# Performance work log

Measured on AMD Instinct MI355X. Metric: run time of the kernel, lower is better.

The kernel has to match this reference:

```python
import jax, jax.numpy as jnp
import numpy as np


def setup_inputs() -> dict:
    key = jax.random.key(0)
    ks = jax.random.split(key, 12)
    B, C, H, W = 8, 256, 64, 64
    inter = C // 8
    s = 0.05  # weight scale keeps q.k logits in a stable softmax range
    f32 = jnp.float32
    x = jax.random.normal(ks[0], (B, C, H, W), f32)
    Wq = jax.random.normal(ks[1], (inter, C), f32) * s
    bq = jnp.zeros((inter,), f32)
    Wk = jax.random.normal(ks[2], (inter, C), f32) * s
    bk = jnp.zeros((inter,), f32)
    Wv = jax.random.normal(ks[3], (C, C), f32) * s
    bv = jnp.zeros((C,), f32)
    gamma = jnp.full((1,), 0.5, f32)  # learnable residual scale (init 0 in torch; 0.5 exercises the path)
    Wg1 = jax.random.normal(ks[4], (inter, C), f32) * s
    bg1 = jnp.zeros((inter,), f32)
    Wg2 = jax.random.normal(ks[5], (C, inter), f32) * s
    bg2 = jnp.zeros((C,), f32)
    return {"x": x, "Wq": Wq, "bq": bq, "Wk": Wk, "bk": bk, "Wv": Wv, "bv": bv,
            "gamma": gamma, "Wg1": Wg1, "bg1": bg1, "Wg2": Wg2, "bg2": bg2}


def reference(x, Wq, bq, Wk, bk, Wv, bv, gamma, Wg1, bg1, Wg2, bg2):
    B, C, H, W = x.shape
    N = H * W
    xf = x.reshape(B, C, N)  # [B,C,N]
    # 1x1 convs == per-pixel linear projections
    q = jnp.einsum('oc,bcn->bon', Wq, xf) + bq[None, :, None]  # [B,inter,N]
    k = jnp.einsum('oc,bcn->bon', Wk, xf) + bk[None, :, None]  # [B,inter,N]
    v = jnp.einsum('oc,bcn->bon', Wv, xf) + bv[None, :, None]  # [B,C,N]
    # attention[b,n,m] = softmax_m( q[b,:,n] . k[b,:,m] )
    attn = jax.nn.softmax(jnp.einsum('bin,bim->bnm', q, k), axis=-1)  # [B,N,N]
    # out[b,c,n] = sum_m v[b,c,m] * attn[b,n,m]
    out = jnp.einsum('bcm,bnm->bcn', v, attn)  # [B,C,N]
    out = gamma[0] * out + xf
    # gated global pooling branch: GAP -> 1x1 conv -> ReLU -> 1x1 conv -> Sigmoid
    gp = xf.mean(axis=-1)  # [B,C]
    h = jax.nn.relu(jnp.einsum('oc,bc->bo', Wg1, gp) + bg1)  # [B,inter]
    ga = jax.nn.sigmoid(jnp.einsum('co,bo->bc', Wg2, h) + bg2)  # [B,C]
    out = out * ga[:, :, None] + out
    return out.reshape(B, C, H, W)
```

## Files before the change

### kernel.cpp

```cpp
#include <hip/hip_runtime.h>

typedef unsigned short u16;
typedef unsigned int   u32;
typedef short s16x4 __attribute__((ext_vector_type(4)));
typedef u16 u16x4 __attribute__((ext_vector_type(4)));
typedef u16 u16x8 __attribute__((ext_vector_type(8)));
typedef __bf16 bf16x8 __attribute__((ext_vector_type(8)));
typedef float f32x4 __attribute__((ext_vector_type(4)));
typedef float f32x2 __attribute__((ext_vector_type(2)));
typedef u32 u32x2v __attribute__((ext_vector_type(2)));
typedef u32 u32x4v __attribute__((ext_vector_type(4)));

#define NB 8
#define NC 256
#define NI 32
#define NN 4096
#define LOG2E 1.4426950408889634f
#define POFF 64.0f

#define OW_Q   0
#define OB_Q   8192
#define OW_K   8224
#define OB_K   16416
#define OW_V   16448
#define OB_V   81984
#define OGAM   82240
#define OW_G1  82248
#define OB_G1  90440
#define OW_G2  90472
#define OB_G2  98664
#define WTOT   98920

__device__ __forceinline__ float bf2f(u16 v) {
    u32 u = ((u32)v) << 16;
    return __builtin_bit_cast(float, u);
}
__device__ __forceinline__ u16 f2bf(float f) {
    u32 u = __builtin_bit_cast(u32, f);
    u32 lsb = (u >> 16) & 1u;
    u += 0x7fffu + lsb;
    return (u16)(u >> 16);
}
__device__ __forceinline__ u32 cvtpk_bf16(float lo, float hi) {
    u32 r;
    asm("v_cvt_pk_bf16_f32 %0, %1, %2" : "=v"(r) : "v"(lo), "v"(hi));
    return r;
}
__device__ __forceinline__ u16 f2bf_hw(float f) {
    u32 r;
    asm("v_cvt_pk_bf16_f32 %0, %1, %1" : "=v"(r) : "v"(f));
    return (u16)r;
}
__device__ __forceinline__ void permswap32(u32& a, u32& b) {
#if __has_builtin(__builtin_amdgcn_permlane32_swap)
    auto r = __builtin_amdgcn_permlane32_swap(a, b, false, false);
    a = (u32)r[0]; b = (u32)r[1];
#else
    int ln = (int)(threadIdx.x & 63);
    u32 a2 = (u32)__shfl_xor((int)a, 32, 64);
    u32 b2 = (u32)__shfl_xor((int)b, 32, 64);
    u32 na = (ln < 32) ? a : b2;
    u32 nb = (ln < 32) ? a2 : b;
    a = na; b = nb;
#endif
}
__device__ __forceinline__ void permswap16(u32& a, u32& b) {
#if __has_builtin(__builtin_amdgcn_permlane16_swap)
    auto r = __builtin_amdgcn_permlane16_swap(a, b, false, false);
    a = (u32)r[0]; b = (u32)r[1];
#else
    int q = (int)((threadIdx.x >> 4) & 1);
    u32 az = (u32)__shfl_xor((int)a, 16, 64);
    u32 bz = (u32)__shfl_xor((int)b, 16, 64);
    u32 na = q ? bz : a;
    u32 nb = q ? b  : az;
    a = na; b = nb;
#endif
}
__device__ __forceinline__ bool is_f32_mode(const void* graw) {
    return ((const u16*)graw)[0] == 0;
}

__global__ __launch_bounds__(256) void convert_kernel(
    const void* x,  const void* Wq, const void* bq, const void* Wk, const void* bk,
    const void* Wv, const void* bv, const void* gamma, const void* Wg1, const void* bg1,
    const void* Wg2, const void* bg2, float* __restrict__ xf, float* __restrict__ wbuf,
    u16* __restrict__ wbf, float* __restrict__ gp)
{
    bool f32m = is_f32_mode(gamma);
    int blk = blockIdx.x, t = threadIdx.x;
    if (blk < 2048) {
        int base = blk * 4096 + t * 16;
        float s = 0.f;
        if (f32m) {
            const float* xs = (const float*)x;
#pragma unroll
            for (int k = 0; k < 4; ++k) {
                f32x4 a = *(const f32x4*)(xs + base + k * 4);
                s += (a[0] + a[1]) + (a[2] + a[3]);
            }
        } else {
            const u16* xs = (const u16*)x;
#pragma unroll
            for (int k = 0; k < 2; ++k) {
                u16x8 a = *(const u16x8*)(xs + base + k * 8);
                f32x4 lo, hi;
#pragma unroll
                for (int j = 0; j < 4; ++j) { lo[j] = bf2f(a[j]); hi[j] = bf2f(a[4 + j]); }
                *(f32x4*)(xf + base + k * 8)     = lo;
                *(f32x4*)(xf + base + k * 8 + 4) = hi;
                s += (lo[0]+lo[1])+(lo[2]+lo[3]) + (hi[0]+hi[1])+(hi[2]+hi[3]);
            }
        }
#pragma unroll
        for (int off = 1; off <= 32; off <<= 1) s += __shfl_xor(s, off, 64);
        __shared__ float ws[4];
        if ((t & 63) == 0) ws[t >> 6] = s;
        __syncthreads();
        if (t == 0) gp[blk] = (ws[0] + ws[1] + ws[2] + ws[3]) * (1.0f / NN);
        return;
    }
    if (blk < 2080) {
        int tid = (blk - 2048) * 256 + t;
        const int off[12] = {OW_Q, OB_Q, OW_K, OB_K, OW_V, OB_V, OGAM, OW_G1, OB_G1, OW_G2, OB_G2, WTOT};
        const int len[11] = {8192, 32, 8192, 32, 65536, 256, 1, 8192, 32, 8192, 256};
        const void* srcs[11] = {Wq, bq, Wk, bk, Wv, bv, gamma, Wg1, bg1, Wg2, bg2};
        for (int w = tid; w < WTOT; w += 32 * 256) {
            int seg = 0;
#pragma unroll
            for (int i = 1; i < 11; ++i) if (w >= off[i]) seg = i;
            int idx = w - off[seg];
            float val = 0.f;
            if (idx < len[seg])
                val = f32m ? ((const float*)srcs[seg])[idx] : bf2f(((const u16*)srcs[seg])[idx]);
            wbuf[w] = val;
        }
        return;
    }
    int tid = (blk - 2080) * 256 + t;
    for (int w = tid; w < 320 * 256; w += 10 * 256) {
        int row = w >> 8, c = w & 255;
        const void* src; int idx; float scale = 1.f;
        if (row < 32)      { src = Wq; idx = row * 256 + c; scale = LOG2E; }
        else if (row < 64) { src = Wk; idx = (row - 32) * 256 + c; }
        else               { src = Wv; idx = (row - 64) * 256 + c; }
        float val = f32m ? ((const float*)src)[idx] : bf2f(((const u16*)src)[idx]);
        wbf[w] = f2bf(val * scale);
    }
}

__global__ __launch_bounds__(256) void proj_kernel(
    const void* xr, const float* __restrict__ xf, const void* graw,
    const float* __restrict__ wbuf, const u16* __restrict__ wbf,
    u16* __restrict__ qt, u16* __restrict__ kt, u16* __restrict__ v)
{
    __shared__ __attribute__((aligned(16))) u16 xs[64][264];

    const float* X = is_f32_mode(graw) ? (const float*)xr : xf;

    int t    = threadIdx.x;
    int lane = t & 63;
    int wave = t >> 6;
    int b    = blockIdx.x >> 6;
    int m0   = (blockIdx.x & 63) << 6;
    int l15  = lane & 15;
    int quad = lane >> 4;

    {
        const float* xb = X + (size_t)b * NC * NN + m0 + lane;
        int c0 = wave * 64;
#pragma unroll
        for (int ci = 0; ci < 64; ci += 4) {
            int c = c0 + ci;
            float a0 = xb[(size_t)(c    ) * NN];
            float a1 = xb[(size_t)(c + 1) * NN];
            float a2 = xb[(size_t)(c + 2) * NN];
            float a3 = xb[(size_t)(c + 3) * NN];
            u32x2v p2;
            p2.x = cvtpk_bf16(a0, a1);
            p2.y = cvtpk_bf16(a2, a3);
            *(u32x2v*)&xs[lane][c] = p2;
        }
    }
    __syncthreads();

    const f32x4 zero4 = {};
    f32x4 acc[5][4];
#pragma unroll
    for (int i = 0; i < 5; ++i)
#pragma unroll
        for (int mt = 0; mt < 4; ++mt) acc[i][mt] = zero4;

    int obase = wave * 80;
    const u16* wb = wbf + (size_t)(obase + l15) * 256 + quad * 8;

    bf16x8 af[5];
#pragma unroll
    for (int i = 0; i < 5; ++i)
        af[i] = *(const bf16x8*)(wb + (size_t)(i * 16) * 256);

#pragma unroll
    for (int kc = 0; kc < 8; ++kc) {
        bf16x8 afn[5], bfr[4];
        if (kc < 7) {
#pragma unroll
            for (int i = 0; i < 5; ++i)
                afn[i] = *(const bf16x8*)(wb + (size_t)(i * 16) * 256 + (kc + 1) * 32);
        }
#pragma unroll
        for (int mt = 0; mt < 4; ++mt)
            bfr[mt] = *(const bf16x8*)&xs[mt * 16 + l15][kc * 32 + quad * 8];
#pragma unroll
        for (int i = 0; i < 5; ++i)
#pragma unroll
            for (int mt = 0; mt < 4; ++mt)
                acc[i][mt] = __builtin_amdgcn_mfma_f32_16x16x32_bf16(af[i], bfr[mt], acc[i][mt], 0, 0, 0);
        if (kc < 7) {
#pragma unroll
            for (int i = 0; i < 5; ++i) af[i] = afn[i];
        }
    }

    __syncthreads();

    if (wave == 0) {
#pragma unroll
        for (int i = 0; i < 4; ++i) {
#pragma unroll
            for (int mt = 0; mt < 4; ++mt) {
                float tv[4];
#pragma unroll
                for (int r = 0; r < 4; ++r) {
                    int o = i * 16 + quad * 4 + r;
                    float bias = (o < 32) ? LOG2E * wbuf[OB_Q + o] : wbuf[OB_K + o - 32];
                    tv[r] = acc[i][mt][r] + bias;
                }
                u32x2v p2;
                p2.x = cvtpk_bf16(tv[0], tv[1]);
                p2.y = cvtpk_bf16(tv[2], tv[3]);
                *(u32x2v*)&xs[mt * 16 + l15][i * 16 + quad * 4] = p2;
            }
        }
        int m = m0 + lane;
        u16* qrow = qt + (size_t)(b * NN + m) * NI;
        u16* krow = kt + (size_t)(b * NN + m) * NI;
#pragma unroll
        for (int j = 0; j < 4; ++j) *(u16x8*)(qrow + j * 8) = *(const u16x8*)&xs[lane][j * 8];
#pragma unroll
        for (int j = 0; j < 4; ++j) *(u16x8*)(krow + j * 8) = *(const u16x8*)&xs[lane][32 + j * 8];
#pragma unroll
        for (int mt = 0; mt < 4; ++mt) {
#pragma unroll
            for (int r = 0; r < 4; ++r) {
                int c = quad * 4 + r;
                v[(size_t)(b * NC + c) * NN + m0 + mt * 16 + l15] = f2bf_hw(acc[4][mt][r] + wbuf[OB_V + c]);
            }
        }
    } else {
#pragma unroll
        for (int i = 0; i < 5; ++i) {
#pragma unroll
            for (int mt = 0; mt < 4; ++mt) {
#pragma unroll
                for (int r = 0; r < 4; ++r) {
                    int c = wave * 80 + i * 16 + quad * 4 + r - 64;
                    v[(size_t)(b * NC + c) * NN + m0 + mt * 16 + l15] = f2bf_hw(acc[i][mt][r] + wbuf[OB_V + c]);
                }
            }
        }
    }
}

__global__ __launch_bounds__(256) void gate_kernel(
    const float* __restrict__ gp, const float* __restrict__ wbuf, float* __restrict__ gmul)
{
    int b = blockIdx.x;
    int t = threadIdx.x;
    __shared__ float gps[NC];
    __shared__ float hs[NI];
    gps[t] = gp[b * NC + t];
    __syncthreads();
    if (t < NI) {
        float a = wbuf[OB_G1 + t];
        for (int c = 0; c < NC; ++c) a += wbuf[OW_G1 + t * NC + c] * gps[c];
        hs[t] = a > 0.f ? a : 0.f;
    }
    __syncthreads();
    float a = wbuf[OB_G2 + t];
#pragma unroll
    for (int i = 0; i < NI; ++i) a += wbuf[OW_G2 + t * NI + i] * hs[i];
    float sig = 1.f / (1.f + __expf(-a));
    gmul[b * NC + t] = 1.f + sig;
}

__global__ __launch_bounds__(512, 4) void flash_kernel(
    const u16* __restrict__ qt, const u16* __restrict__ kt, const u16* __restrict__ v,
    const void* xr, const float* __restrict__ xf, const void* graw,
    const float* __restrict__ wbuf, const float* __restrict__ gmul, void* outp)
{
    __shared__ __attribute__((aligned(16))) u16 vs[2][2][NC][40];

    bool f32m = is_f32_mode(graw);
    const float* X = f32m ? (const float*)xr : xf;

    int t    = threadIdx.x;
    int lane = t & 63;
    int wave = t >> 6;
    int b    = blockIdx.x & 7;
    int nblk = (blockIdx.x >> 3) << 6;
    int n0   = nblk + (wave >> 2) * 32;
    int c0   = (wave & 3) * 64;
    int l15  = lane & 15;
    int quad = lane >> 4;

    const f32x4 mneg = {-POFF, -POFF, -POFF, -POFF};

    bf16x8 qf[2];
#pragma unroll
    for (int n16 = 0; n16 < 2; ++n16)
        qf[n16] = *(const bf16x8*)(qt + (size_t)(b * NN + n0 + n16 * 16 + l15) * NI + quad * 8);

    f32x4 acc[2][4];
#pragma unroll
    for (int n16 = 0; n16 < 2; ++n16)
#pragma unroll
        for (int ct = 0; ct < 4; ++ct) acc[n16][ct] = f32x4{};
    f32x2 psum2[2] = {};

    int sc = t >> 2;
    int sm = (t & 3) * 8;
    const u16* vb0 = v + (size_t)(b * NC + sc) * NN + sm;
    const u16* vb1 = v + (size_t)(b * NC + sc + 128) * NN + sm;
    const u16* ktb = kt + (size_t)(b * NN + l15) * NI + quad * 8;

    u16x8 sr0, sr1, sr2, sr3;
    sr0 = *(const u16x8*)(vb0);        sr1 = *(const u16x8*)(vb1);
    sr2 = *(const u16x8*)(vb0 + 32);   sr3 = *(const u16x8*)(vb1 + 32);
    *(u16x8*)&vs[0][0][sc][sm]       = sr0;
    *(u16x8*)&vs[0][0][sc + 128][sm] = sr1;
    *(u16x8*)&vs[0][1][sc][sm]       = sr2;
    *(u16x8*)&vs[0][1][sc + 128][sm] = sr3;
    sr0 = *(const u16x8*)(vb0 + 64);   sr1 = *(const u16x8*)(vb1 + 64);
    sr2 = *(const u16x8*)(vb0 + 96);   sr3 = *(const u16x8*)(vb1 + 96);
    bf16x8 ktA[2], ktB[2];
    ktA[0] = *(const bf16x8*)(ktb);
    ktA[1] = *(const bf16x8*)(ktb + (size_t)16 * NI);
    ktB[0] = *(const bf16x8*)(ktb + (size_t)32 * NI);
    ktB[1] = *(const bf16x8*)(ktb + (size_t)48 * NI);
    __syncthreads();

    for (int it = 0; it < 64; ++it) {
        int p = it & 1;
        bool wmore = (it < 63);
        bool lmore = (it < 62);

        if (wmore) {
            *(u16x8*)&vs[p ^ 1][0][sc][sm]       = sr0;
            *(u16x8*)&vs[p ^ 1][0][sc + 128][sm] = sr1;
            *(u16x8*)&vs[p ^ 1][1][sc][sm]       = sr2;
            *(u16x8*)&vs[p ^ 1][1][sc + 128][sm] = sr3;
        }
        if (lmore) {
            int cb = it * 64 + 128;
            sr0 = *(const u16x8*)(vb0 + cb);
            sr1 = *(const u16x8*)(vb1 + cb);
            sr2 = *(const u16x8*)(vb0 + cb + 32);
            sr3 = *(const u16x8*)(vb1 + cb + 32);
        }

#pragma unroll
        for (int h = 0; h < 2; ++h) {
            bf16x8* ktX = (h == 0) ? ktA : ktB;

            f32x4 sf[2][2];
#pragma unroll
            for (int mt = 0; mt < 2; ++mt)
#pragma unroll
                for (int n16 = 0; n16 < 2; ++n16)
                    sf[n16][mt] = __builtin_amdgcn_mfma_f32_16x16x32_bf16(ktX[mt], qf[n16], mneg, 0, 0, 0);

            bf16x8 va8[4];
#pragma unroll
            for (int ct = 0; ct < 4; ++ct)
                va8[ct] = *(const bf16x8*)&vs[p][h][c0 + ct * 16 + l15][quad * 8];

            if (wmore) {
                int mg = it * 64 + 64 + h * 32;
                ktX[0] = *(const bf16x8*)(ktb + (size_t)mg * NI);
                ktX[1] = *(const bf16x8*)(ktb + (size_t)(mg + 16) * NI);
            }

            bf16x8 pfr8[2];
#pragma unroll
            for (int n16 = 0; n16 < 2; ++n16) {
                float pp[2][4];
#pragma unroll
                for (int mt = 0; mt < 2; ++mt)
#pragma unroll
                    for (int r = 0; r < 4; ++r)
                        pp[mt][r] = __builtin_amdgcn_exp2f(sf[n16][mt][r]);
                f32x2 t0; t0.x = pp[0][0]; t0.y = pp[0][1];
                f32x2 t1; t1.x = pp[0][2]; t1.y = pp[0][3];
                f32x2 t2; t2.x = pp[1][0]; t2.y = pp[1][1];
                f32x2 t3; t3.x = pp[1][2]; t3.y = pp[1][3];
                psum2[n16] += (t0 + t1) + (t2 + t3);
                u32 A0 = cvtpk_bf16(pp[0][0], pp[0][1]);
                u32 A1 = cvtpk_bf16(pp[0][2], pp[0][3]);
                u32 B0 = cvtpk_bf16(pp[1][0], pp[1][1]);
                u32 B1 = cvtpk_bf16(pp[1][2], pp[1][3]);
                permswap32(A0, B0); permswap16(A0, B0);
                permswap32(A1, B1); permswap16(A1, B1);
                u32x4v f; f.x = A0; f.y = A1; f.z = B0; f.w = B1;
                pfr8[n16] = __builtin_bit_cast(bf16x8, f);
            }

#pragma unroll
            for (int ct = 0; ct < 4; ++ct)
#pragma unroll
                for (int n16 = 0; n16 < 2; ++n16)
                    acc[n16][ct] = __builtin_amdgcn_mfma_f32_16x16x32_bf16(va8[ct], pfr8[n16], acc[n16][ct], 0, 0, 0);
        }

        __syncthreads();
    }

    float inv[2];
#pragma unroll
    for (int n16 = 0; n16 < 2; ++n16) {
        float s = psum2[n16].x + psum2[n16].y;
        s += __shfl_xor(s, 16, 64);
        s += __shfl_xor(s, 32, 64);
        inv[n16] = 1.f / s;
    }
    float gam = wbuf[OGAM];

#pragma unroll
    for (int n16 = 0; n16 < 2; ++n16) {
        int n = n0 + n16 * 16 + l15;
#pragma unroll
        for (int ct = 0; ct < 4; ++ct) {
            int cb = c0 + ct * 16 + quad * 4;
            f32x4 gm4 = *(const f32x4*)&gmul[b * NC + cb];
#pragma unroll
            for (int r = 0; r < 4; ++r) {
                size_t off = (size_t)(b * NC + cb + r) * NN + n;
                float val = (gam * acc[n16][ct][r] * inv[n16] + X[off]) * gm4[r];
                if (f32m) ((float*)outp)[off] = val;
                else      ((u16*)outp)[off]  = f2bf_hw(val);
            }
        }
    }
}

extern "C" void kernel_launch(void* const* d_in, const int* in_sizes, int n_in,
                              void* d_out, int out_size, void* d_ws, size_t ws_size,
                              hipStream_t stream)
{
    const void* x     = d_in[0];
    const void* Wq    = d_in[1];
    const void* bq    = d_in[2];
    const void* Wk    = d_in[3];
    const void* bk    = d_in[4];
    const void* Wv    = d_in[5];
    const void* bvp   = d_in[6];
    const void* gamma = d_in[7];
    const void* Wg1   = d_in[8];
    const void* bg1   = d_in[9];
    const void* Wg2   = d_in[10];
    const void* bg2   = d_in[11];

    char* ws = (char*)d_ws;
    float* xf   = (float*)ws;
    float* wbuf = (float*)(ws + 33554432);
    u16*   qt   = (u16*)  (ws + 33951744);
    u16*   kt   = (u16*)  (ws + 36048896);
    u16*   v    = (u16*)  (ws + 38146048);
    float* gp   = (float*)(ws + 54923264);
    float* gmul = (float*)(ws + 54931456);
    u16*   wbf  = (u16*)  (ws + 54939648);

    convert_kernel<<<2090, 256, 0, stream>>>(x, Wq, bq, Wk, bk, Wv, bvp, gamma,
                                             Wg1, bg1, Wg2, bg2, xf, wbuf, wbf, gp);
    proj_kernel<<<NB * 64, 256, 0, stream>>>(x, xf, gamma, wbuf, wbf, qt, kt, v);
    gate_kernel<<<NB, 256, 0, stream>>>(gp, wbuf, gmul);
    flash_kernel<<<NB * 64, 512, 0, stream>>>(qt, kt, v, x, xf, gamma, wbuf, gmul, d_out);
}
```

Baseline: 270.0 us.

## Retile flash waves to 16 rows x 128 channels; drop bf16 x staging copy

The flash kernel's per-wave tile changes from 32 query rows by 64 channels to 16 query rows by 128 channels. Each wave now computes one QK score tile per key block instead of two, so exp2, softmax-sum and pack work per wave halves, while each wave reads twice as many V fragments from LDS. Separately, the bf16 path no longer writes an fp32 copy of x in the pooling kernel; the projection and epilogue read bf16 x directly. The inputs here are fp32, so the default run mostly sees the retiling, which trades fewer redundant exponentials for more LDS traffic per wave.

```diff
diff --git a/kernel.cpp b/kernel.cpp
--- a/kernel.cpp
+++ b/kernel.cpp
@@ -104,12 +104,8 @@
 #pragma unroll
             for (int k = 0; k < 2; ++k) {
                 u16x8 a = *(const u16x8*)(xs + base + k * 8);
-                f32x4 lo, hi;
-#pragma unroll
-                for (int j = 0; j < 4; ++j) { lo[j] = bf2f(a[j]); hi[j] = bf2f(a[4 + j]); }
-                *(f32x4*)(xf + base + k * 8)     = lo;
-                *(f32x4*)(xf + base + k * 8 + 4) = hi;
-                s += (lo[0]+lo[1])+(lo[2]+lo[3]) + (hi[0]+hi[1])+(hi[2]+hi[3]);
+#pragma unroll
+                for (int j = 0; j < 8; ++j) s += bf2f(a[j]);
             }
         }
 #pragma unroll
@@ -156,7 +152,7 @@
 {
     __shared__ __attribute__((aligned(16))) u16 xs[64][264];
 
-    const float* X = is_f32_mode(graw) ? (const float*)xr : xf;
+    bool f32m = is_f32_mode(graw);
 
     int t    = threadIdx.x;
     int lane = t & 63;
@@ -167,19 +163,33 @@
     int quad = lane >> 4;
 
     {
-        const float* xb = X + (size_t)b * NC * NN + m0 + lane;
         int c0 = wave * 64;
-#pragma unroll
-        for (int ci = 0; ci < 64; ci += 4) {
-            int c = c0 + ci;
-            float a0 = xb[(size_t)(c    ) * NN];
-            float a1 = xb[(size_t)(c + 1) * NN];
-            float a2 = xb[(size_t)(c + 2) * NN];
-            float a3 = xb[(size_t)(c + 3) * NN];
-            u32x2v p2;
-            p2.x = cvtpk_bf16(a0, a1);
-            p2.y = cvtpk_bf16(a2, a3);
-            *(u32x2v*)&xs[lane][c] = p2;
+        if (f32m) {
+            const float* xb = (const float*)xr + (size_t)b * NC * NN + m0 + lane;
+#pragma unroll
+            for (int ci = 0; ci < 64; ci += 4) {
+                int c = c0 + ci;
+                float a0 = xb[(size_t)(c    ) * NN];
+                float a1 = xb[(size_t)(c + 1) * NN];
+                float a2 = xb[(size_t)(c + 2) * NN];
+                float a3 = xb[(size_t)(c + 3) * NN];
+                u32x2v p2;
+                p2.x = cvtpk_bf16(a0, a1);
+                p2.y = cvtpk_bf16(a2, a3);
+                *(u32x2v*)&xs[lane][c] = p2;
+            }
+        } else {
+            const u16* xb = (const u16*)xr + (size_t)b * NC * NN + m0 + lane;
+#pragma unroll
+            for (int ci = 0; ci < 64; ci += 4) {
+                int c = c0 + ci;
+                u16x4 p4;
+                p4[0] = xb[(size_t)(c    ) * NN];
+                p4[1] = xb[(size_t)(c + 1) * NN];
+                p4[2] = xb[(size_t)(c + 2) * NN];
+                p4[3] = xb[(size_t)(c + 3) * NN];
+                *(u16x4*)&xs[lane][c] = p4;
+            }
         }
     }
     __syncthreads();
@@ -301,31 +311,25 @@
     __shared__ __attribute__((aligned(16))) u16 vs[2][2][NC][40];
 
     bool f32m = is_f32_mode(graw);
-    const float* X = f32m ? (const float*)xr : xf;
 
     int t    = threadIdx.x;
     int lane = t & 63;
     int wave = t >> 6;
     int b    = blockIdx.x & 7;
     int nblk = (blockIdx.x >> 3) << 6;
-    int n0   = nblk + (wave >> 2) * 32;
-    int c0   = (wave & 3) * 64;
+    int n0   = nblk + (wave >> 1) * 16;
+    int c0   = (wave & 1) * 128;
     int l15  = lane & 15;
     int quad = lane >> 4;
 
     const f32x4 mneg = {-POFF, -POFF, -POFF, -POFF};
 
-    bf16x8 qf[2];
-#pragma unroll
-    for (int n16 = 0; n16 < 2; ++n16)
-        qf[n16] = *(const bf16x8*)(qt + (size_t)(b * NN + n0 + n16 * 16 + l15) * NI + quad * 8);
-
-    f32x4 acc[2][4];
-#pragma unroll
-    for (int n16 = 0; n16 < 2; ++n16)
-#pragma unroll
-        for (int ct = 0; ct < 4; ++ct) acc[n16][ct] = f32x4{};
-    f32x2 psum2[2] = {};
+    bf16x8 qf = *(const bf16x8*)(qt + (size_t)(b * NN + n0 + l15) * NI + quad * 8);
+
+    f32x4 acc[8];
+#pragma unroll
+    for (int ct = 0; ct < 8; ++ct) acc[ct] = f32x4{};
+    f32x2 psum2 = {};
 
     int sc = t >> 2;
     int sm = (t & 3) * 8;
@@ -372,16 +376,14 @@
         for (int h = 0; h < 2; ++h) {
             bf16x8* ktX = (h == 0) ? ktA : ktB;
 
-            f32x4 sf[2][2];
+            f32x4 sf[2];
 #pragma unroll
             for (int mt = 0; mt < 2; ++mt)
-#pragma unroll
-                for (int n16 = 0; n16 < 2; ++n16)
-                    sf[n16][mt] = __builtin_amdgcn_mfma_f32_16x16x32_bf16(ktX[mt], qf[n16], mneg, 0, 0, 0);
-
-            bf16x8 va8[4];
-#pragma unroll
-            for (int ct = 0; ct < 4; ++ct)
+                sf[mt] = __builtin_amdgcn_mfma_f32_16x16x32_bf16(ktX[mt], qf, mneg, 0, 0, 0);
+
+            bf16x8 va8[8];
+#pragma unroll
+            for (int ct = 0; ct < 8; ++ct)
                 va8[ct] = *(const bf16x8*)&vs[p][h][c0 + ct * 16 + l15][quad * 8];
 
             if (wmore) {
@@ -390,64 +392,52 @@
                 ktX[1] = *(const bf16x8*)(ktb + (size_t)(mg + 16) * NI);
             }
 
-            bf16x8 pfr8[2];
-#pragma unroll
-            for (int n16 = 0; n16 < 2; ++n16) {
-                float pp[2][4];
-#pragma unroll
-                for (int mt = 0; mt < 2; ++mt)
-#pragma unroll
-                    for (int r = 0; r < 4; ++r)
-                        pp[mt][r] = __builtin_amdgcn_exp2f(sf[n16][mt][r]);
-                f32x2 t0; t0.x = pp[0][0]; t0.y = pp[0][1];
-                f32x2 t1; t1.x = pp[0][2]; t1.y = pp[0][3];
-                f32x2 t2; t2.x = pp[1][0]; t2.y = pp[1][1];
-                f32x2 t3; t3.x = pp[1][2]; t3.y = pp[1][3];
-                psum2[n16] += (t0 + t1) + (t2 + t3);
-                u32 A0 = cvtpk_bf16(pp[0][0], pp[0][1]);
-                u32 A1 = cvtpk_bf16(pp[0][2], pp[0][3]);
-                u32 B0 = cvtpk_bf16(pp[1][0], pp[1][1]);
-                u32 B1 = cvtpk_bf16(pp[1][2], pp[1][3]);
-                permswap32(A0, B0); permswap16(A0, B0);
-                permswap32(A1, B1); permswap16(A1, B1);
-                u32x4v f; f.x = A0; f.y = A1; f.z = B0; f.w = B1;
-                pfr8[n16] = __builtin_bit_cast(bf16x8, f);
-            }
-
-#pragma unroll
-            for (int ct = 0; ct < 4; ++ct)
-#pragma unroll
-                for (int n16 = 0; n16 < 2; ++n16)
-                    acc[n16][ct] = __builtin_amdgcn_mfma_f32_16x16x32_bf16(va8[ct], pfr8[n16], acc[n16][ct], 0, 0, 0);
+            float pp[2][4];
+#pragma unroll
+            for (int mt = 0; mt < 2; ++mt)
+#pragma unroll
+                for (int r = 0; r < 4; ++r)
+                    pp[mt][r] = __builtin_amdgcn_exp2f(sf[mt][r]);
+            f32x2 t0; t0.x = pp[0][0]; t0.y = pp[0][1];
+            f32x2 t1; t1.x = pp[0][2]; t1.y = pp[0][3];
+            f32x2 t2; t2.x = pp[1][0]; t2.y = pp[1][1];
+            f32x2 t3; t3.x = pp[1][2]; t3.y = pp[1][3];
+            psum2 += (t0 + t1) + (t2 + t3);
+            u32 A0 = cvtpk_bf16(pp[0][0], pp[0][1]);
+            u32 A1 = cvtpk_bf16(pp[0][2], pp[0][3]);
+            u32 B0 = cvtpk_bf16(pp[1][0], pp[1][1]);
+            u32 B1 = cvtpk_bf16(pp[1][2], pp[1][3]);
+            permswap32(A0, B0); permswap16(A0, B0);
+            permswap32(A1, B1); permswap16(A1, B1);
+            u32x4v f; f.x = A0; f.y = A1; f.z = B0; f.w = B1;
+            bf16x8 pfr8 = __builtin_bit_cast(bf16x8, f);
+
+#pragma unroll
+            for (int ct = 0; ct < 8; ++ct)
+                acc[ct] = __builtin_amdgcn_mfma_f32_16x16x32_bf16(va8[ct], pfr8, acc[ct], 0, 0, 0);
         }
 
         __syncthreads();
     }
 
-    float inv[2];
-#pragma unroll
-    for (int n16 = 0; n16 < 2; ++n16) {
-        float s = psum2[n16].x + psum2[n16].y;
-        s += __shfl_xor(s, 16, 64);
-        s += __shfl_xor(s, 32, 64);
-        inv[n16] = 1.f / s;
-    }
+    float s = psum2.x + psum2.y;
+    s += __shfl_xor(s, 16, 64);
+    s += __shfl_xor(s, 32, 64);
+    float inv = 1.f / s;
     float gam = wbuf[OGAM];
-
-#pragma unroll
-    for (int n16 = 0; n16 < 2; ++n16) {
-        int n = n0 + n16 * 16 + l15;
-#pragma unroll
-        for (int ct = 0; ct < 4; ++ct) {
-            int cb = c0 + ct * 16 + quad * 4;
-            f32x4 gm4 = *(const f32x4*)&gmul[b * NC + cb];
-#pragma unroll
-            for (int r = 0; r < 4; ++r) {
-                size_t off = (size_t)(b * NC + cb + r) * NN + n;
-                float val = (gam * acc[n16][ct][r] * inv[n16] + X[off]) * gm4[r];
-                if (f32m) ((float*)outp)[off] = val;
-                else      ((u16*)outp)[off]  = f2bf_hw(val);
-            }
+    int n = n0 + l15;
+
+#pragma unroll
+    for (int ct = 0; ct < 8; ++ct) {
+        int cb = c0 + ct * 16 + quad * 4;
+        f32x4 gm4 = *(const f32x4*)&gmul[b * NC + cb];
+#pragma unroll
+        for (int r = 0; r < 4; ++r) {
+            size_t off = (size_t)(b * NC + cb + r) * NN + n;
+            float xv = f32m ? ((const float*)xr)[off] : bf2f(((const u16*)xr)[off]);
+            float val = (gam * acc[ct][r] * inv + xv) * gm4[r];
+            if (f32m) ((float*)outp)[off] = val;
+            else      ((u16*)outp)[off]  = f2bf_hw(val);
         }
     }
 }
```

New measurement: 257.9 us. 1.05x faster.

## Split key halves across waves to cut redundant softmax work, reduce partials via LDS

Applied to the files above, without the earlier changes.

Repartitions flash-attention waves so each wave handles one 32-key half and 128 channels instead of both halves and 64 channels. This halves the duplicated QK MFMA and exp2 work per wave, and a shared-memory reduction merges the partial accumulators and denominators at the end. It also removes the bf16-to-f32 staging copy of x, so later kernels read bf16 input directly. In exchange, accumulator registers double, which may pressure occupancy, and an extra LDS epilogue is added.

```diff
diff --git a/kernel.cpp b/kernel.cpp
--- a/kernel.cpp
+++ b/kernel.cpp
@@ -104,12 +104,8 @@
 #pragma unroll
             for (int k = 0; k < 2; ++k) {
                 u16x8 a = *(const u16x8*)(xs + base + k * 8);
-                f32x4 lo, hi;
-#pragma unroll
-                for (int j = 0; j < 4; ++j) { lo[j] = bf2f(a[j]); hi[j] = bf2f(a[4 + j]); }
-                *(f32x4*)(xf + base + k * 8)     = lo;
-                *(f32x4*)(xf + base + k * 8 + 4) = hi;
-                s += (lo[0]+lo[1])+(lo[2]+lo[3]) + (hi[0]+hi[1])+(hi[2]+hi[3]);
+#pragma unroll
+                for (int j = 0; j < 8; ++j) s += bf2f(a[j]);
             }
         }
 #pragma unroll
@@ -156,7 +152,7 @@
 {
     __shared__ __attribute__((aligned(16))) u16 xs[64][264];
 
-    const float* X = is_f32_mode(graw) ? (const float*)xr : xf;
+    bool f32m = is_f32_mode(graw);
 
     int t    = threadIdx.x;
     int lane = t & 63;
@@ -167,19 +163,33 @@
     int quad = lane >> 4;
 
     {
-        const float* xb = X + (size_t)b * NC * NN + m0 + lane;
         int c0 = wave * 64;
-#pragma unroll
-        for (int ci = 0; ci < 64; ci += 4) {
-            int c = c0 + ci;
-            float a0 = xb[(size_t)(c    ) * NN];
-            float a1 = xb[(size_t)(c + 1) * NN];
-            float a2 = xb[(size_t)(c + 2) * NN];
-            float a3 = xb[(size_t)(c + 3) * NN];
-            u32x2v p2;
-            p2.x = cvtpk_bf16(a0, a1);
-            p2.y = cvtpk_bf16(a2, a3);
-            *(u32x2v*)&xs[lane][c] = p2;
+        if (f32m) {
+            const float* xb = (const float*)xr + (size_t)b * NC * NN + m0 + lane;
+#pragma unroll
+            for (int ci = 0; ci < 64; ci += 4) {
+                int c = c0 + ci;
+                float a0 = xb[(size_t)(c    ) * NN];
+                float a1 = xb[(size_t)(c + 1) * NN];
+                float a2 = xb[(size_t)(c + 2) * NN];
+                float a3 = xb[(size_t)(c + 3) * NN];
+                u32x2v p2;
+                p2.x = cvtpk_bf16(a0, a1);
+                p2.y = cvtpk_bf16(a2, a3);
+                *(u32x2v*)&xs[lane][c] = p2;
+            }
+        } else {
+            const u16* xb = (const u16*)xr + (size_t)b * NC * NN + m0 + lane;
+#pragma unroll
+            for (int ci = 0; ci < 64; ci += 4) {
+                int c = c0 + ci;
+                u16x4 p4;
+                p4[0] = xb[(size_t)(c    ) * NN];
+                p4[1] = xb[(size_t)(c + 1) * NN];
+                p4[2] = xb[(size_t)(c + 2) * NN];
+                p4[3] = xb[(size_t)(c + 3) * NN];
+                *(u16x4*)&xs[lane][c] = p4;
+            }
         }
     }
     __syncthreads();
@@ -301,15 +311,17 @@
     __shared__ __attribute__((aligned(16))) u16 vs[2][2][NC][40];
 
     bool f32m = is_f32_mode(graw);
-    const float* X = f32m ? (const float*)xr : xf;
 
     int t    = threadIdx.x;
     int lane = t & 63;
     int wave = t >> 6;
+    int mg   = wave & 1;
+    int cg   = (wave >> 1) & 1;
+    int ng   = wave >> 2;
     int b    = blockIdx.x & 7;
     int nblk = (blockIdx.x >> 3) << 6;
-    int n0   = nblk + (wave >> 2) * 32;
-    int c0   = (wave & 3) * 64;
+    int n0   = nblk + ng * 32;
+    int c0   = cg * 128;
     int l15  = lane & 15;
     int quad = lane >> 4;
 
@@ -320,11 +332,11 @@
     for (int n16 = 0; n16 < 2; ++n16)
         qf[n16] = *(const bf16x8*)(qt + (size_t)(b * NN + n0 + n16 * 16 + l15) * NI + quad * 8);
 
-    f32x4 acc[2][4];
+    f32x4 acc[2][8];
 #pragma unroll
     for (int n16 = 0; n16 < 2; ++n16)
 #pragma unroll
-        for (int ct = 0; ct < 4; ++ct) acc[n16][ct] = f32x4{};
+        for (int ct = 0; ct < 8; ++ct) acc[n16][ct] = f32x4{};
     f32x2 psum2[2] = {};
 
     int sc = t >> 2;
@@ -342,11 +354,9 @@
     *(u16x8*)&vs[0][1][sc + 128][sm] = sr3;
     sr0 = *(const u16x8*)(vb0 + 64);   sr1 = *(const u16x8*)(vb1 + 64);
     sr2 = *(const u16x8*)(vb0 + 96);   sr3 = *(const u16x8*)(vb1 + 96);
-    bf16x8 ktA[2], ktB[2];
-    ktA[0] = *(const bf16x8*)(ktb);
-    ktA[1] = *(const bf16x8*)(ktb + (size_t)16 * NI);
-    ktB[0] = *(const bf16x8*)(ktb + (size_t)32 * NI);
-    ktB[1] = *(const bf16x8*)(ktb + (size_t)48 * NI);
+    bf16x8 ktA[2];
+    ktA[0] = *(const bf16x8*)(ktb + (size_t)(mg * 32     ) * NI);
+    ktA[1] = *(const bf16x8*)(ktb + (size_t)(mg * 32 + 16) * NI);
     __syncthreads();
 
     for (int it = 0; it < 64; ++it) {
@@ -368,85 +378,101 @@
             sr3 = *(const u16x8*)(vb1 + cb + 32);
         }
 
-#pragma unroll
-        for (int h = 0; h < 2; ++h) {
-            bf16x8* ktX = (h == 0) ? ktA : ktB;
-
-            f32x4 sf[2][2];
+        f32x4 sf[2][2];
+#pragma unroll
+        for (int mt = 0; mt < 2; ++mt)
+#pragma unroll
+            for (int n16 = 0; n16 < 2; ++n16)
+                sf[n16][mt] = __builtin_amdgcn_mfma_f32_16x16x32_bf16(ktA[mt], qf[n16], mneg, 0, 0, 0);
+
+        if (wmore) {
+            int mgn = (it + 1) * 64 + mg * 32;
+            ktA[0] = *(const bf16x8*)(ktb + (size_t)(mgn     ) * NI);
+            ktA[1] = *(const bf16x8*)(ktb + (size_t)(mgn + 16) * NI);
+        }
+
+        bf16x8 pfr8[2];
+#pragma unroll
+        for (int n16 = 0; n16 < 2; ++n16) {
+            float pp[2][4];
 #pragma unroll
             for (int mt = 0; mt < 2; ++mt)
 #pragma unroll
-                for (int n16 = 0; n16 < 2; ++n16)
-                    sf[n16][mt] = __builtin_amdgcn_mfma_f32_16x16x32_bf16(ktX[mt], qf[n16], mneg, 0, 0, 0);
-
-            bf16x8 va8[4];
-#pragma unroll
-            for (int ct = 0; ct < 4; ++ct)
-                va8[ct] = *(const bf16x8*)&vs[p][h][c0 + ct * 16 + l15][quad * 8];
-
-            if (wmore) {
-                int mg = it * 64 + 64 + h * 32;
-                ktX[0] = *(const bf16x8*)(ktb + (size_t)mg * NI);
-                ktX[1] = *(const bf16x8*)(ktb + (size_t)(mg + 16) * NI);
-            }
-
-            bf16x8 pfr8[2];
-#pragma unroll
-            for (int n16 = 0; n16 < 2; ++n16) {
-                float pp[2][4];
-#pragma unroll
-                for (int mt = 0; mt < 2; ++mt)
-#pragma unroll
-                    for (int r = 0; r < 4; ++r)
-                        pp[mt][r] = __builtin_amdgcn_exp2f(sf[n16][mt][r]);
-                f32x2 t0; t0.x = pp[0][0]; t0.y = pp[0][1];
-                f32x2 t1; t1.x = pp[0][2]; t1.y = pp[0][3];
-                f32x2 t2; t2.x = pp[1][0]; t2.y = pp[1][1];
-                f32x2 t3; t3.x = pp[1][2]; t3.y = pp[1][3];
-                psum2[n16] += (t0 + t1) + (t2 + t3);
-                u32 A0 = cvtpk_bf16(pp[0][0], pp[0][1]);
-                u32 A1 = cvtpk_bf16(pp[0][2], pp[0][3]);
-                u32 B0 = cvtpk_bf16(pp[1][0], pp[1][1]);
-                u32 B1 = cvtpk_bf16(pp[1][2], pp[1][3]);
-                permswap32(A0, B0); permswap16(A0, B0);
-                permswap32(A1, B1); permswap16(A1, B1);
-                u32x4v f; f.x = A0; f.y = A1; f.z = B0; f.w = B1;
-                pfr8[n16] = __builtin_bit_cast(bf16x8, f);
-            }
-
-#pragma unroll
-            for (int ct = 0; ct < 4; ++ct)
-#pragma unroll
-                for (int n16 = 0; n16 < 2; ++n16)
-                    acc[n16][ct] = __builtin_amdgcn_mfma_f32_16x16x32_bf16(va8[ct], pfr8[n16], acc[n16][ct], 0, 0, 0);
+                for (int r = 0; r < 4; ++r)
+                    pp[mt][r] = __builtin_amdgcn_exp2f(sf[n16][mt][r]);
+            f32x2 t0; t0.x = pp[0][0]; t0.y = pp[0][1];
+            f32x2 t1; t1.x = pp[0][2]; t1.y = pp[0][3];
+            f32x2 t2; t2.x = pp[1][0]; t2.y = pp[1][1];
+            f32x2 t3; t3.x = pp[1][2]; t3.y = pp[1][3];
+            psum2[n16] += (t0 + t1) + (t2 + t3);
+            u32 A0 = cvtpk_bf16(pp[0][0], pp[0][1]);
+            u32 A1 = cvtpk_bf16(pp[0][2], pp[0][3]);
+            u32 B0 = cvtpk_bf16(pp[1][0], pp[1][1]);
+            u32 B1 = cvtpk_bf16(pp[1][2], pp[1][3]);
+            permswap32(A0, B0); permswap16(A0, B0);
+            permswap32(A1, B1); permswap16(A1, B1);
+            u32x4v f; f.x = A0; f.y = A1; f.z = B0; f.w = B1;
+            pfr8[n16] = __builtin_bit_cast(bf16x8, f);
+        }
+
+#pragma unroll
+        for (int ct = 0; ct < 8; ++ct) {
+            bf16x8 va = *(const bf16x8*)&vs[p][mg][c0 + ct * 16 + l15][quad * 8];
+            acc[0][ct] = __builtin_amdgcn_mfma_f32_16x16x32_bf16(va, pfr8[0], acc[0][ct], 0, 0, 0);
+            acc[1][ct] = __builtin_amdgcn_mfma_f32_16x16x32_bf16(va, pfr8[1], acc[1][ct], 0, 0, 0);
         }
 
         __syncthreads();
     }
 
-    float inv[2];
+    float* sbuf = (float*)&vs[0][0][0][0];
+    float* dlp  = (float*)((char*)&vs[0][0][0][0] + 70656);
+    int pid = wave >> 1;
+
+    float sden[2];
 #pragma unroll
     for (int n16 = 0; n16 < 2; ++n16) {
         float s = psum2[n16].x + psum2[n16].y;
         s += __shfl_xor(s, 16, 64);
         s += __shfl_xor(s, 32, 64);
-        inv[n16] = 1.f / s;
-    }
-    float gam = wbuf[OGAM];
-
-#pragma unroll
-    for (int n16 = 0; n16 < 2; ++n16) {
-        int n = n0 + n16 * 16 + l15;
-#pragma unroll
-        for (int ct = 0; ct < 4; ++ct) {
-            int cb = c0 + ct * 16 + quad * 4;
-            f32x4 gm4 = *(const f32x4*)&gmul[b * NC + cb];
-#pragma unroll
-            for (int r = 0; r < 4; ++r) {
-                size_t off = (size_t)(b * NC + cb + r) * NN + n;
-                float val = (gam * acc[n16][ct][r] * inv[n16] + X[off]) * gm4[r];
-                if (f32m) ((float*)outp)[off] = val;
-                else      ((u16*)outp)[off]  = f2bf_hw(val);
+        sden[n16] = s;
+    }
+    if (quad == 0) {
+        dlp[(wave * 2 + 0) * 16 + l15] = sden[0];
+        dlp[(wave * 2 + 1) * 16 + l15] = sden[1];
+    }
+    if (mg == 1) {
+#pragma unroll
+        for (int n16 = 0; n16 < 2; ++n16)
+#pragma unroll
+            for (int ct = 0; ct < 8; ++ct)
+                *(f32x4*)&sbuf[pid * 4352 + lane * 68 + n16 * 32 + ct * 4] = acc[n16][ct];
+    }
+    __syncthreads();
+    if (mg == 0) {
+        float inv[2];
+#pragma unroll
+        for (int n16 = 0; n16 < 2; ++n16)
+            inv[n16] = 1.f / (dlp[(wave * 2 + n16) * 16 + l15] +
+                              dlp[((wave + 1) * 2 + n16) * 16 + l15]);
+        float gam = wbuf[OGAM];
+#pragma unroll
+        for (int n16 = 0; n16 < 2; ++n16) {
+            int n = n0 + n16 * 16 + l15;
+#pragma unroll
+            for (int ct = 0; ct < 8; ++ct) {
+                f32x4 part = *(const f32x4*)&sbuf[pid * 4352 + lane * 68 + n16 * 32 + ct * 4];
+                int cb = c0 + ct * 16 + quad * 4;
+                f32x4 gm4 = *(const f32x4*)&gmul[b * NC + cb];
+#pragma unroll
+                for (int r = 0; r < 4; ++r) {
+                    size_t off = (size_t)(b * NC + cb + r) * NN + n;
+                    float a  = acc[n16][ct][r] + part[r];
+                    float xv = f32m ? ((const float*)xr)[off] : bf2f(((const u16*)xr)[off]);
+                    float val = (gam * a * inv[n16] + xv) * gm4[r];
+                    if (f32m) ((float*)outp)[off] = val;
+                    else      ((u16*)outp)[off]  = f2bf_hw(val);
+                }
             }
         }
     }
```

Result: slower. 279.6 us (+3.5%).
